# Optimization experiments

Hardware: AMD Instinct MI355X
Metric: run time of the kernel (lower is better)

The kernel has to match this reference:

```python
import jax, jax.numpy as jnp
import numpy as np

N_NODES = 100000
N_EDGES = 1600000
D = 128
L = 3
BN_EPS = 1e-5


def setup_inputs() -> dict:
    key = jax.random.key(0)
    ks = jax.random.split(key, 6)
    x = jax.random.normal(ks[0], (N_NODES, D), dtype=jnp.float32)
    edge_index = jax.random.randint(ks[1], (2, N_EDGES), 0, N_NODES, dtype=jnp.int64)
    Wl = jax.random.normal(ks[2], (L, D, D), dtype=jnp.float32) / np.sqrt(D)
    bl = jax.random.normal(ks[3], (L, D), dtype=jnp.float32) * 0.01
    Wr = jax.random.normal(ks[4], (L, D, D), dtype=jnp.float32) / np.sqrt(D)
    gamma = jnp.ones((L, D), dtype=jnp.float32)
    beta = jnp.zeros((L, D), dtype=jnp.float32)
    return {"x": x, "edge_index": edge_index, "Wl": Wl, "bl": bl,
            "Wr": Wr, "gamma": gamma, "beta": beta}


def _sage_layer(x, src, dst, inv_deg, Wl_i, bl_i, Wr_i, gamma_i, beta_i):
    # mean aggregation over incoming edges: scatter-add messages then divide by degree
    agg_sum = jax.ops.segment_sum(x[src], dst, num_segments=N_NODES)  # [N, D]
    agg = agg_sum * inv_deg[:, None]
    # SAGEConv: lin_l(agg) (with bias) + lin_r(x) (no bias)
    h = jnp.einsum('nd,hd->nh', agg, Wl_i) + bl_i + jnp.einsum('nd,hd->nh', x, Wr_i)
    # BatchNorm1d (training-mode batch stats, biased variance)
    mean = jnp.mean(h, axis=0)
    var = jnp.mean(jnp.square(h - mean), axis=0)
    h = (h - mean) * jax.lax.rsqrt(var + BN_EPS) * gamma_i + beta_i
    return jax.nn.relu(h)  # dropout is identity in eval mode


def reference(x, edge_index, Wl, bl, Wr, gamma, beta):
    src, dst = edge_index[0], edge_index[1]
    deg = jax.ops.segment_sum(jnp.ones((N_EDGES,), jnp.float32), dst,
                              num_segments=N_NODES)
    inv_deg = 1.0 / jnp.maximum(deg, 1.0)
    for i in range(L):
        h = _sage_layer(x, src, dst, inv_deg, Wl[i], bl[i], Wr[i], gamma[i], beta[i])
        if 0 < i < L - 1:  # middle layers get a scaled residual (shapes match)
            x = x + 0.5 * h
        else:
            x = h
    return x
```

## Files before the change

kernel.cpp:

```cpp
#include <hip/hip_runtime.h>

#define N_NODES 100000
#define N_EDGES 1600000
#define D 128
#define BN_EPS 1e-5f
#define N_GB ((N_NODES + 63) / 64)
#define NPART 8
#define FILL_BLOCKS 2048
#define NODES_PER_PART (N_NODES / NPART)
#define CAP 48
#define PCAP 210000

typedef short bf16x8 __attribute__((ext_vector_type(8)));
typedef float f32x4 __attribute__((ext_vector_type(4)));

__device__ inline unsigned short f32_to_bf16_rne(float f) {
    unsigned u = __builtin_bit_cast(unsigned, f);
    u += 0x7fffu + ((u >> 16) & 1u);
    return (unsigned short)(u >> 16);
}
__device__ inline float bf16lo_to_f32(unsigned v) { return __builtin_bit_cast(float, v << 16); }
__device__ inline float bf16hi_to_f32(unsigned v) { return __builtin_bit_cast(float, v & 0xffff0000u); }

__device__ inline void gload_lds16(const void* g, void* l) {
    __builtin_amdgcn_global_load_lds((const __attribute__((address_space(1))) unsigned*)g,
                                     (__attribute__((address_space(3))) unsigned*)l, 16, 0, 0);
}


__global__ __launch_bounds__(256) void k_prep(const float* __restrict__ x_in,
                                              const float* __restrict__ Wl, const float* __restrict__ Wr,
                                              unsigned short* __restrict__ xhi,
                                              unsigned short* __restrict__ wl_hi, unsigned short* __restrict__ wl_lo,
                                              unsigned short* __restrict__ wr_hi, unsigned short* __restrict__ wr_lo,
                                              int* __restrict__ cursor, int* __restrict__ gcur) {
    for (int idx = blockIdx.x * 256 + threadIdx.x; idx < N_NODES * 32; idx += FILL_BLOCKS * 256) {
        float4 v = ((const float4*)x_in)[idx];
        uint2 p;
        p.x = (unsigned)f32_to_bf16_rne(v.x) | ((unsigned)f32_to_bf16_rne(v.y) << 16);
        p.y = (unsigned)f32_to_bf16_rne(v.z) | ((unsigned)f32_to_bf16_rne(v.w) << 16);
        ((uint2*)xhi)[idx] = p;
    }
    for (int i = blockIdx.x * 256 + threadIdx.x; i < 2 * 3 * D * D; i += FILL_BLOCKS * 256) {
        const float* srcp = (i < 3 * D * D) ? Wl : Wr;
        int j = (i < 3 * D * D) ? i : i - 3 * D * D;
        float w = srcp[j];
        unsigned short h = f32_to_bf16_rne(w);
        float rem = w - bf16lo_to_f32((unsigned)h);
        if (i < 3 * D * D) { wl_hi[j] = h; wl_lo[j] = f32_to_bf16_rne(rem); }
        else               { wr_hi[j] = h; wr_lo[j] = f32_to_bf16_rne(rem); }
    }
    for (int i = blockIdx.x * 256 + threadIdx.x; i < N_NODES; i += FILL_BLOCKS * 256)
        cursor[i] = 0;
    if (blockIdx.x == 0 && threadIdx.x < NPART) gcur[threadIdx.x] = 0;
}

__global__ __launch_bounds__(256) void k_split(const int* __restrict__ src, const int* __restrict__ dst,
                                               int* __restrict__ gcur, unsigned* __restrict__ pairbuf) {
    __shared__ int cnt[NPART];
    __shared__ int base[NPART];
    const int t = threadIdx.x;
    if (t < NPART) cnt[t] = 0;
    __syncthreads();
    unsigned pk[4];
    int part[4], pos[4];
    const int e0 = blockIdx.x * 256 + t;
#pragma unroll
    for (int r = 0; r < 4; r++) {
        int e = e0 + r * (FILL_BLOCKS * 256);
        part[r] = -1;
        if (e < N_EDGES) {
            int d = dst[e];
            int s = src[e];
            int p = d / NODES_PER_PART;
            part[r] = p;
            pos[r] = atomicAdd(&cnt[p], 1);
            pk[r] = ((unsigned)(d - p * NODES_PER_PART) << 17) | (unsigned)s;
        }
    }
    __syncthreads();
    if (t < NPART) base[t] = atomicAdd(&gcur[t], cnt[t]);
    __syncthreads();
#pragma unroll
    for (int r = 0; r < 4; r++) {
        if (part[r] >= 0) {
            unsigned idx = (unsigned)(base[part[r]] + pos[r]);
            if (idx < PCAP) pairbuf[(size_t)part[r] * PCAP + idx] = pk[r];
        }
    }
}

__global__ __launch_bounds__(256) void k_fill2(const unsigned* __restrict__ pairbuf,
                                               const int* __restrict__ gcur,
                                               int* __restrict__ cursor, int* __restrict__ colidx) {
    const int p = blockIdx.x & (NPART - 1);
    const int m = gcur[p];
    const int stride = (FILL_BLOCKS / NPART) * 256;
    const unsigned* pb = pairbuf + (size_t)p * PCAP;
    const int dbase = p * NODES_PER_PART;
    for (int i = (blockIdx.x >> 3) * 256 + threadIdx.x; i < m; i += stride) {
        unsigned pk = pb[i];
        int d = dbase + (int)(pk >> 17);
        int pos = atomicAdd(&cursor[d], 1);
        if (pos < CAP) colidx[d * CAP + pos] = (int)(pk & 0x1FFFFu);
    }
}


__global__ __launch_bounds__(256) void k_agg(const unsigned short* __restrict__ xhi,
                                             const int* __restrict__ cursor, const int* __restrict__ colidx,
                                             unsigned short* __restrict__ agghi) {
    const int wid = threadIdx.x >> 6;
    const int l = threadIdx.x & 63;
    const int n = blockIdx.x * 4 + wid;
    if (n >= N_NODES) return;
    const int degree = cursor[n];
    const int b = n * CAP;
    const int e = b + (degree < CAP ? degree : CAP);
    const int c8 = l & 15;
    const int g = l >> 4;
    const size_t coff = (size_t)c8 * 16;

    float acc[8];
#pragma unroll
    for (int k = 0; k < 8; k++) acc[k] = 0.f;

    int i = b;
    while (i < e) {
        int chunk = e - i; if (chunk > 64) chunk = 64;
        int myE = colidx[i + (l < chunk ? l : chunk - 1)];
        int j = 0;
        for (; j + 8 <= chunk; j += 8) {
            int s0 = __shfl(myE, j + g);
            int s1 = __shfl(myE, j + 4 + g);
            uint4 v0 = *(const uint4*)((const char*)xhi + (size_t)s0 * 256 + coff);
            uint4 v1 = *(const uint4*)((const char*)xhi + (size_t)s1 * 256 + coff);
            acc[0] += bf16lo_to_f32(v0.x); acc[1] += bf16hi_to_f32(v0.x);
            acc[2] += bf16lo_to_f32(v0.y); acc[3] += bf16hi_to_f32(v0.y);
            acc[4] += bf16lo_to_f32(v0.z); acc[5] += bf16hi_to_f32(v0.z);
            acc[6] += bf16lo_to_f32(v0.w); acc[7] += bf16hi_to_f32(v0.w);
            acc[0] += bf16lo_to_f32(v1.x); acc[1] += bf16hi_to_f32(v1.x);
            acc[2] += bf16lo_to_f32(v1.y); acc[3] += bf16hi_to_f32(v1.y);
            acc[4] += bf16lo_to_f32(v1.z); acc[5] += bf16hi_to_f32(v1.z);
            acc[6] += bf16lo_to_f32(v1.w); acc[7] += bf16hi_to_f32(v1.w);
        }
        for (; j + 4 <= chunk; j += 4) {
            int s0 = __shfl(myE, j + g);
            uint4 v0 = *(const uint4*)((const char*)xhi + (size_t)s0 * 256 + coff);
            acc[0] += bf16lo_to_f32(v0.x); acc[1] += bf16hi_to_f32(v0.x);
            acc[2] += bf16lo_to_f32(v0.y); acc[3] += bf16hi_to_f32(v0.y);
            acc[4] += bf16lo_to_f32(v0.z); acc[5] += bf16hi_to_f32(v0.z);
            acc[6] += bf16lo_to_f32(v0.w); acc[7] += bf16hi_to_f32(v0.w);
        }
        if (j < chunk) {
            int idx = j + g;
            int s0 = __shfl(myE, idx < chunk ? idx : chunk - 1);
            if (idx < chunk) {
                uint4 v0 = *(const uint4*)((const char*)xhi + (size_t)s0 * 256 + coff);
                acc[0] += bf16lo_to_f32(v0.x); acc[1] += bf16hi_to_f32(v0.x);
                acc[2] += bf16lo_to_f32(v0.y); acc[3] += bf16hi_to_f32(v0.y);
                acc[4] += bf16lo_to_f32(v0.z); acc[5] += bf16hi_to_f32(v0.z);
                acc[6] += bf16lo_to_f32(v0.w); acc[7] += bf16hi_to_f32(v0.w);
            }
        }
        i += chunk;
    }
#pragma unroll
    for (int k = 0; k < 8; k++) {
        acc[k] += __shfl_xor(acc[k], 16);
        acc[k] += __shfl_xor(acc[k], 32);
    }
    if (g == 0) {
        float idg = 1.0f / fmaxf((float)degree, 1.0f);
        uint4 p;
        p.x = (unsigned)f32_to_bf16_rne(acc[0] * idg) | ((unsigned)f32_to_bf16_rne(acc[1] * idg) << 16);
        p.y = (unsigned)f32_to_bf16_rne(acc[2] * idg) | ((unsigned)f32_to_bf16_rne(acc[3] * idg) << 16);
        p.z = (unsigned)f32_to_bf16_rne(acc[4] * idg) | ((unsigned)f32_to_bf16_rne(acc[5] * idg) << 16);
        p.w = (unsigned)f32_to_bf16_rne(acc[6] * idg) | ((unsigned)f32_to_bf16_rne(acc[7] * idg) << 16);
        *(uint4*)((char*)agghi + (size_t)n * 256 + coff) = p;
    }
}

__global__ __launch_bounds__(256, 2) void k_gemm(
    const unsigned short* __restrict__ agg_hi, const unsigned short* __restrict__ x_hi,
    const unsigned short* __restrict__ wl_hi, const unsigned short* __restrict__ wl_lo,
    const unsigned short* __restrict__ wr_hi, const unsigned short* __restrict__ wr_lo,
    const float* __restrict__ bl, unsigned short* __restrict__ h, float* __restrict__ partial) {
    __shared__ char lds[32768];
    const int t = threadIdx.x;
    const int w = t >> 6;
    const int l = t & 63;
    const int lr = l & 15;
    const int lg = l >> 4;
    const int base = blockIdx.x * 64;
    const int j0 = w * 32;

    {
#pragma unroll
        for (int i = 0; i < 8; i++) {
            int c = w * 8 + i;
            int ci = c & 15;
            int m = ci >> 2, kk = ci & 3;
            int n = base + m * 16 + lr;
            if (n > N_NODES - 1) n = N_NODES - 1;
            size_t goff = (size_t)n * 256 + kk * 64 + lg * 16;
            const char* srcp = ((c & 16) ? (const char*)x_hi : (const char*)agg_hi) + goff;
            gload_lds16(srcp, lds + c * 1024);
        }
    }

    f32x4 acc[4][2];
#pragma unroll
    for (int m = 0; m < 4; m++)
#pragma unroll
        for (int f = 0; f < 2; f++) acc[m][f] = (f32x4){0.f, 0.f, 0.f, 0.f};

#pragma unroll
    for (int seg = 0; seg < 2; seg++) {
        const unsigned short* WH = seg ? wr_hi : wl_hi;
        const unsigned short* WLo = seg ? wr_lo : wl_lo;
        bf16x8 wh[4][2], wlo[4][2];
#pragma unroll
        for (int kk = 0; kk < 4; kk++)
#pragma unroll
            for (int f = 0; f < 2; f++) {
                size_t wo = (size_t)(j0 + f * 16 + lr) * D + kk * 32 + lg * 8;
                wh[kk][f] = *(const bf16x8*)(WH + wo);
                wlo[kk][f] = *(const bf16x8*)(WLo + wo);
            }
        asm volatile("" :: "v"(wh[0][0]), "v"(wh[0][1]), "v"(wh[1][0]), "v"(wh[1][1]),
                           "v"(wh[2][0]), "v"(wh[2][1]), "v"(wh[3][0]), "v"(wh[3][1]));
        asm volatile("" :: "v"(wlo[0][0]), "v"(wlo[0][1]), "v"(wlo[1][0]), "v"(wlo[1][1]),
                           "v"(wlo[2][0]), "v"(wlo[2][1]), "v"(wlo[3][0]), "v"(wlo[3][1]));
        if (seg == 0) __syncthreads();
        const int tb = seg * 16384;
#pragma unroll
        for (int kk = 0; kk < 4; kk++) {
            bf16x8 a[4];
#pragma unroll
            for (int m = 0; m < 4; m++)
                a[m] = *(const bf16x8*)(lds + tb + (m * 4 + kk) * 1024 + l * 16);
#pragma unroll
            for (int f = 0; f < 2; f++)
#pragma unroll
                for (int m = 0; m < 4; m++) {
                    acc[m][f] = __builtin_amdgcn_mfma_f32_16x16x32_bf16(a[m], wh[kk][f], acc[m][f], 0, 0, 0);
                    acc[m][f] = __builtin_amdgcn_mfma_f32_16x16x32_bf16(a[m], wlo[kk][f], acc[m][f], 0, 0, 0);
                }
        }
    }

    float s1[2] = {0.f, 0.f}, s2[2] = {0.f, 0.f};
#pragma unroll
    for (int f = 0; f < 2; f++) {
        const int col = j0 + f * 16 + lr;
        const float bias = bl[col];
#pragma unroll
        for (int m = 0; m < 4; m++) {
#pragma unroll
            for (int r = 0; r < 4; r++) {
                int n = base + m * 16 + lg * 4 + r;
                if (n < N_NODES) {
                    float v = acc[m][f][r] + bias;
                    h[(size_t)n * D + col] = f32_to_bf16_rne(v);
                    s1[f] += v;
                    s2[f] += v * v;
                }
            }
        }
    }
#pragma unroll
    for (int f = 0; f < 2; f++) {
        s1[f] += __shfl_xor(s1[f], 16);
        s1[f] += __shfl_xor(s1[f], 32);
        s2[f] += __shfl_xor(s2[f], 16);
        s2[f] += __shfl_xor(s2[f], 32);
    }
    if (l < 16) {
        float* pp = partial + (size_t)blockIdx.x * 256;
        pp[j0 + l] = s1[0];
        pp[j0 + 16 + l] = s1[1];
        pp[128 + j0 + l] = s2[0];
        pp[128 + j0 + 16 + l] = s2[1];
    }
}

__global__ __launch_bounds__(256) void k_bnred(const float* __restrict__ partial, float* __restrict__ bn32) {
    int t = threadIdx.x;
    float s = 0.f;
    for (int b = blockIdx.x; b < N_GB; b += 32)
        s += partial[(size_t)b * 256 + t];
    bn32[blockIdx.x * 256 + t] = s;
}

__global__ __launch_bounds__(256) void k_apply(const unsigned short* __restrict__ h,
                                               const float* __restrict__ bn32,
                                               const float* __restrict__ gamma, const float* __restrict__ beta,
                                               const unsigned short* __restrict__ xres_hi,
                                               unsigned short* __restrict__ out_hi,
                                               float* __restrict__ out_f32, int mode) {
    __shared__ float sa[128], sc[128];
    int t = threadIdx.x;
    if (t < 128) {
        float m1 = 0.f, m2 = 0.f;
#pragma unroll 8
        for (int i = 0; i < 32; i++) {
            m1 += bn32[i * 256 + t];
            m2 += bn32[i * 256 + 128 + t];
        }
        float mean = m1 * (1.0f / N_NODES);
        float var = m2 * (1.0f / N_NODES) - mean * mean;
        float inv = rsqrtf(var + BN_EPS);
        float av = gamma[t] * inv;
        sa[t] = av;
        sc[t] = beta[t] - mean * av;
    }
    __syncthreads();
    int idx = blockIdx.x * 256 + t;
    if (idx >= N_NODES * 32) return;
    int c0 = (idx & 31) * 4;
    uint2 hv = ((const uint2*)h)[idx];
    float r0 = fmaxf(fmaf(bf16lo_to_f32(hv.x), sa[c0], sc[c0]), 0.f);
    float r1 = fmaxf(fmaf(bf16hi_to_f32(hv.x), sa[c0 + 1], sc[c0 + 1]), 0.f);
    float r2 = fmaxf(fmaf(bf16lo_to_f32(hv.y), sa[c0 + 2], sc[c0 + 2]), 0.f);
    float r3 = fmaxf(fmaf(bf16hi_to_f32(hv.y), sa[c0 + 3], sc[c0 + 3]), 0.f);
    if (mode == 1) {
        uint2 xv = ((const uint2*)xres_hi)[idx];
        r0 = fmaf(0.5f, r0, bf16lo_to_f32(xv.x));
        r1 = fmaf(0.5f, r1, bf16hi_to_f32(xv.x));
        r2 = fmaf(0.5f, r2, bf16lo_to_f32(xv.y));
        r3 = fmaf(0.5f, r3, bf16hi_to_f32(xv.y));
    }
    if (mode == 2) {
        ((float4*)out_f32)[idx] = make_float4(r0, r1, r2, r3);
    } else {
        uint2 p;
        p.x = (unsigned)f32_to_bf16_rne(r0) | ((unsigned)f32_to_bf16_rne(r1) << 16);
        p.y = (unsigned)f32_to_bf16_rne(r2) | ((unsigned)f32_to_bf16_rne(r3) << 16);
        ((uint2*)out_hi)[idx] = p;
    }
}


extern "C" void kernel_launch(void* const* d_in, const int* in_sizes, int n_in,
                              void* d_out, int out_size, void* d_ws, size_t ws_size,
                              hipStream_t stream) {
    const float* x_in = (const float*)d_in[0];
    const int* ei = (const int*)d_in[1];
    const float* Wl = (const float*)d_in[2];
    const float* bl = (const float*)d_in[3];
    const float* Wr = (const float*)d_in[4];
    const float* gamma = (const float*)d_in[5];
    const float* beta = (const float*)d_in[6];
    float* out = (float*)d_out;

    char* ws = (char*)d_ws;
    unsigned short* xhiA = (unsigned short*)ws; ws += (size_t)N_NODES * D * 2;
    unsigned short* xhiB = (unsigned short*)ws; ws += (size_t)N_NODES * D * 2;
    unsigned short* agghi = (unsigned short*)ws; ws += (size_t)N_NODES * D * 2;
    int* cursor = (int*)ws; ws += (size_t)N_NODES * 4;
    int* colidx = (int*)ws; ws += (size_t)N_NODES * CAP * 4;
    unsigned* pairbuf = (unsigned*)ws; ws += (size_t)NPART * PCAP * 4;
    int* gcur = (int*)ws; ws += 64;
    unsigned short* wl_hi = (unsigned short*)ws; ws += (size_t)3 * D * D * 2;
    unsigned short* wl_lo = (unsigned short*)ws; ws += (size_t)3 * D * D * 2;
    unsigned short* wr_hi = (unsigned short*)ws; ws += (size_t)3 * D * D * 2;
    unsigned short* wr_lo = (unsigned short*)ws; ws += (size_t)3 * D * D * 2;
    float* partial = (float*)ws; ws += (size_t)N_GB * 256 * 4;
    float* bn32 = (float*)ws; ws += 32 * 256 * 4;

    const int* src = ei;
    const int* dst = ei + N_EDGES;

    k_prep<<<FILL_BLOCKS, 256, 0, stream>>>(x_in, Wl, Wr, xhiA, wl_hi, wl_lo, wr_hi, wr_lo,
                                            cursor, gcur);
    k_split<<<FILL_BLOCKS, 256, 0, stream>>>(src, dst, gcur, pairbuf);
    k_fill2<<<FILL_BLOCKS, 256, 0, stream>>>(pairbuf, gcur, cursor, colidx);

    unsigned short* xin[3] = { xhiA, xhiB, xhiA };
    unsigned short* xout[3] = { xhiB, xhiA, (unsigned short*)0 };
    int mode[3] = { 0, 1, 2 };

    for (int i = 0; i < 3; i++) {
        k_agg<<<(N_NODES + 3) / 4, 256, 0, stream>>>(xin[i], cursor, colidx, agghi);
        k_gemm<<<N_GB, 256, 0, stream>>>(agghi, xin[i],
                                         wl_hi + (size_t)i * D * D, wl_lo + (size_t)i * D * D,
                                         wr_hi + (size_t)i * D * D, wr_lo + (size_t)i * D * D,
                                         bl + (size_t)i * D, agghi, partial);
        k_bnred<<<32, 256, 0, stream>>>(partial, bn32);
        k_apply<<<(N_NODES * 32 + 255) / 256, 256, 0, stream>>>(agghi, bn32,
                                                                gamma + (size_t)i * D, beta + (size_t)i * D,
                                                                xin[i], xout[i], out, mode[i]);
    }
}
```

Before: 526.1 us.

## Build CSR buckets in shared memory per node chunk instead of global atomics

Replaces the global-atomic adjacency fill with a kernel where each block owns a 250-node chunk of a partition, scans the whole partition's pair buffer, buckets matching edges with LDS atomics, then writes colidx and cursor with coalesced vector stores. This removes the cursor zeroing from the prep kernel and avoids scattered global atomics. In exchange, every block rereads the full partition buffer, multiplying read traffic, and LDS use limits occupancy.

New measurement: 675.3 us. 1.28x slower.

```diff
diff --git a/kernel.cpp b/kernel.cpp
--- a/kernel.cpp
+++ b/kernel.cpp
@@ -10,6 +10,8 @@
 #define NODES_PER_PART (N_NODES / NPART)
 #define CAP 48
 #define PCAP 210000
+#define NPB 250
+#define FILL3_BLOCKS (NPART * 50)
 
 typedef short bf16x8 __attribute__((ext_vector_type(8)));
 typedef float f32x4 __attribute__((ext_vector_type(4)));
@@ -33,7 +35,7 @@
                                               unsigned short* __restrict__ xhi,
                                               unsigned short* __restrict__ wl_hi, unsigned short* __restrict__ wl_lo,
                                               unsigned short* __restrict__ wr_hi, unsigned short* __restrict__ wr_lo,
-                                              int* __restrict__ cursor, int* __restrict__ gcur) {
+                                              int* __restrict__ gcur) {
     for (int idx = blockIdx.x * 256 + threadIdx.x; idx < N_NODES * 32; idx += FILL_BLOCKS * 256) {
         float4 v = ((const float4*)x_in)[idx];
         uint2 p;
@@ -50,8 +52,6 @@
         if (i < 3 * D * D) { wl_hi[j] = h; wl_lo[j] = f32_to_bf16_rne(rem); }
         else               { wr_hi[j] = h; wr_lo[j] = f32_to_bf16_rne(rem); }
     }
-    for (int i = blockIdx.x * 256 + threadIdx.x; i < N_NODES; i += FILL_BLOCKS * 256)
-        cursor[i] = 0;
     if (blockIdx.x == 0 && threadIdx.x < NPART) gcur[threadIdx.x] = 0;
 }
 
@@ -90,20 +90,36 @@
     }
 }
 
-__global__ __launch_bounds__(256) void k_fill2(const unsigned* __restrict__ pairbuf,
+__global__ __launch_bounds__(256) void k_fill3(const unsigned* __restrict__ pairbuf,
                                                const int* __restrict__ gcur,
                                                int* __restrict__ cursor, int* __restrict__ colidx) {
+    __shared__ int lcnt[NPB];
+    __shared__ int lbuf[NPB * CAP];
+    const int t = threadIdx.x;
     const int p = blockIdx.x & (NPART - 1);
-    const int m = gcur[p];
-    const int stride = (FILL_BLOCKS / NPART) * 256;
+    const int c = blockIdx.x >> 3;
+    const int nbase = c * NPB;
+    const int gbase = p * NODES_PER_PART + nbase;
+
+    for (int i = t; i < NPB; i += 256) lcnt[i] = 0;
+    __syncthreads();
+
+    int m = gcur[p]; if (m > PCAP) m = PCAP;
     const unsigned* pb = pairbuf + (size_t)p * PCAP;
-    const int dbase = p * NODES_PER_PART;
-    for (int i = (blockIdx.x >> 3) * 256 + threadIdx.x; i < m; i += stride) {
+    for (int i = t; i < m; i += 256) {
         unsigned pk = pb[i];
-        int d = dbase + (int)(pk >> 17);
-        int pos = atomicAdd(&cursor[d], 1);
-        if (pos < CAP) colidx[d * CAP + pos] = (int)(pk & 0x1FFFFu);
-    }
+        int r = (int)(pk >> 17) - nbase;
+        if ((unsigned)r < NPB) {
+            int pos = atomicAdd(&lcnt[r], 1);
+            if (pos < CAP) lbuf[r * CAP + pos] = (int)(pk & 0x1FFFFu);
+        }
+    }
+    __syncthreads();
+
+    uint4* dst4 = (uint4*)(colidx + (size_t)gbase * CAP);
+    const uint4* src4 = (const uint4*)lbuf;
+    for (int s4 = t; s4 < NPB * CAP / 4; s4 += 256) dst4[s4] = src4[s4];
+    for (int i = t; i < NPB; i += 256) cursor[gbase + i] = lcnt[i];
 }
 
 
@@ -372,10 +388,9 @@
     const int* src = ei;
     const int* dst = ei + N_EDGES;
 
-    k_prep<<<FILL_BLOCKS, 256, 0, stream>>>(x_in, Wl, Wr, xhiA, wl_hi, wl_lo, wr_hi, wr_lo,
-                                            cursor, gcur);
+    k_prep<<<FILL_BLOCKS, 256, 0, stream>>>(x_in, Wl, Wr, xhiA, wl_hi, wl_lo, wr_hi, wr_lo, gcur);
     k_split<<<FILL_BLOCKS, 256, 0, stream>>>(src, dst, gcur, pairbuf);
-    k_fill2<<<FILL_BLOCKS, 256, 0, stream>>>(pairbuf, gcur, cursor, colidx);
+    k_fill3<<<FILL3_BLOCKS, 256, 0, stream>>>(pairbuf, gcur, cursor, colidx);
 
     unsigned short* xin[3] = { xhiA, xhiB, xhiA };
     unsigned short* xout[3] = { xhiB, xhiA, (unsigned short*)0 };
```
